# Optimization experiments

Measured on AMD Instinct MI355X. Metric: run time of the kernel, lower is better.

## Reference

```python
import jax, jax.numpy as jnp
import numpy as np

N_NODES = 100000
N_EDGES = 1600000
D = 128


def sage_conv(x, src, dst, W_l, b_l, W_r):
    # mean aggregation of neighbor features: messages flow src -> dst
    msgs = x[src]                                           # [E, D] gather
    agg = jax.ops.segment_sum(msgs, dst, num_segments=x.shape[0])  # [N, D]
    deg = jax.ops.segment_sum(jnp.ones((src.shape[0],), x.dtype), dst,
                              num_segments=x.shape[0])       # [N]
    agg = agg / jnp.maximum(deg, 1.0)[:, None]
    # PyG SAGEConv: lin_l(aggregated) + lin_r(root); bias lives in lin_l
    return agg @ W_l.T + b_l + x @ W_r.T


def setup_inputs() -> dict:
    key = jax.random.key(0)
    ks = jax.random.split(key, 8)
    s = 1.0 / np.sqrt(D)
    return {
        "x": jax.random.normal(ks[0], (N_NODES, D), dtype=jnp.float32),
        "edge_index": jax.random.randint(ks[1], (2, N_EDGES), 0, N_NODES, dtype=jnp.int64),
        "W1_l": jax.random.normal(ks[2], (D, D), dtype=jnp.float32) * s,
        "b1": jnp.zeros((D,), dtype=jnp.float32),
        "W1_r": jax.random.normal(ks[3], (D, D), dtype=jnp.float32) * s,
        "W2_l": jax.random.normal(ks[4], (D, D), dtype=jnp.float32) * s,
        "b2": jnp.zeros((D,), dtype=jnp.float32),
        "W2_r": jax.random.normal(ks[5], (D, D), dtype=jnp.float32) * s,
    }


def reference(x, edge_index, W1_l, b1, W1_r, W2_l, b2, W2_r):
    src, dst = edge_index[0], edge_index[1]
    h = jax.nn.relu(sage_conv(x, src, dst, W1_l, b1, W1_r))
    out = sage_conv(h, src, dst, W2_l, b2, W2_r)
    return out
```

## Files before the change

kernel.cpp:

```cpp
#include <hip/hip_runtime.h>
#include <cstdint>
#include <cstddef>

#define D 128

typedef unsigned short ushort_t;
typedef unsigned int uint_t;
typedef __attribute__((ext_vector_type(8))) short bf16x8;
typedef __attribute__((ext_vector_type(4))) float f32x4;

static __device__ __forceinline__ unsigned short f2bf(float f) {
    unsigned int u = __float_as_uint(f);
    u = (u + 0x7FFFu + ((u >> 16) & 1u)) >> 16;
    return (unsigned short)u;
}
static __device__ __forceinline__ float bf_lo(uint_t v) {
    return __uint_as_float(v << 16);
}
static __device__ __forceinline__ float bf_hi(uint_t v) {
    return __uint_as_float(v & 0xFFFF0000u);
}

static __device__ __forceinline__ void cast8(const float* __restrict__ s,
                                             ushort_t* __restrict__ d) {
    float4 a = *(const float4*)s;
    float4 b = *(const float4*)(s + 4);
    uint4 o;
    o.x = (uint_t)f2bf(a.x) | ((uint_t)f2bf(a.y) << 16);
    o.y = (uint_t)f2bf(a.z) | ((uint_t)f2bf(a.w) << 16);
    o.z = (uint_t)f2bf(b.x) | ((uint_t)f2bf(b.y) << 16);
    o.w = (uint_t)f2bf(b.z) | ((uint_t)f2bf(b.w) << 16);
    *(uint4*)d = o;
}


__global__ __launch_bounds__(256) void front_fused(
    const int* __restrict__ dst, int* __restrict__ bhist, int E, int EB,
    const float* __restrict__ x, ushort_t* __restrict__ xb, long nx, int CX,
    const float* __restrict__ W1l, const float* __restrict__ W1r,
    const float* __restrict__ W2l, const float* __restrict__ W2r,
    ushort_t* __restrict__ W1lb, ushort_t* __restrict__ W1rb,
    ushort_t* __restrict__ W2lb, ushort_t* __restrict__ W2rb) {
    __shared__ int lh[512];
    int b = blockIdx.x, t = threadIdx.x;
    if (b < EB) {
        lh[t] = 0;
        lh[t + 256] = 0;
        __syncthreads();
        int base = b * 4096;
#pragma unroll
        for (int i = 0; i < 16; ++i) {
            int e = base + i * 256 + t;
            if (e < E) atomicAdd(&lh[dst[e] >> 8], 1);
        }
        __syncthreads();
        if (lh[t]) atomicAdd(&bhist[t], lh[t]);
        if (lh[t + 256]) atomicAdd(&bhist[t + 256], lh[t + 256]);
    } else if (b < EB + CX) {
        long i = ((long)(b - EB) * 256 + t) * 8;
        if (i < nx) cast8(x + i, xb + i);
    } else {
        int bb = b - EB - CX;
        int arr = bb >> 3;
        long i = ((long)(bb & 7) * 256 + t) * 8;
        const float* s = (arr == 0) ? W1l : (arr == 1) ? W1r
                       : (arr == 2) ? W2l : W2r;
        ushort_t* d = (arr == 0) ? W1lb : (arr == 1) ? W1rb
                    : (arr == 2) ? W2lb : W2rb;
        cast8(s + i, d + i);
    }
}


__global__ __launch_bounds__(512) void bkt_scan(const int* __restrict__ bhist,
                                                int* __restrict__ boff,
                                                int* __restrict__ bcur,
                                                int* __restrict__ row_ptr,
                                                int N, int E) {
    __shared__ int s[512];
    int t = threadIdx.x;
    int v = bhist[t];
    s[t] = v;
    __syncthreads();
    for (int off = 1; off < 512; off <<= 1) {
        int u = (t >= off) ? s[t - off] : 0;
        __syncthreads();
        s[t] += u;
        __syncthreads();
    }
    int ex = s[t] - v;
    boff[t] = ex;
    bcur[t] = ex;
    if (t == 511) boff[512] = s[511];
    if (t == 0) row_ptr[N] = E;
}

__global__ __launch_bounds__(256) void bkt_scatter(const int* __restrict__ src,
                                                   const int* __restrict__ dst,
                                                   int* __restrict__ bcur,
                                                   int* __restrict__ ebuf, int E) {
    __shared__ int lh[512];
    __shared__ int lofs[512];
    __shared__ int gb[512];
    __shared__ int sv[4096];
    __shared__ unsigned short sb[4096];
    int t = threadIdx.x;
    lh[t] = 0;
    lh[t + 256] = 0;
    __syncthreads();
    int base = blockIdx.x * 4096;
    unsigned pk[16];
#pragma unroll
    for (int i = 0; i < 16; ++i) {
        int e = base + i * 256 + t;
        unsigned p = 0xFFFFFFFFu;
        if (e < E) {
            int d = dst[e];
            int bkt = d >> 8;
            int r = atomicAdd(&lh[bkt], 1);
            p = ((unsigned)r << 17) | ((unsigned)bkt << 8) | (unsigned)(d & 255);
        }
        pk[i] = p;
    }
    __syncthreads();
    int a0 = lh[2 * t], a1 = lh[2 * t + 1];
    int ps = a0 + a1;
    gb[t] = ps;
    __syncthreads();
    for (int off = 1; off < 256; off <<= 1) {
        int u = (t >= off) ? gb[t - off] : 0;
        __syncthreads();
        gb[t] += u;
        __syncthreads();
    }
    int inc = gb[t];
    int exb = inc - ps;
    __syncthreads();
    lofs[2 * t] = exb;
    lofs[2 * t + 1] = exb + a0;
    if (a0) gb[2 * t] = atomicAdd(&bcur[2 * t], a0);
    if (a1) gb[2 * t + 1] = atomicAdd(&bcur[2 * t + 1], a1);
    __syncthreads();
#pragma unroll
    for (int i = 0; i < 16; ++i) {
        int e = base + i * 256 + t;
        if (e < E) {
            unsigned p = pk[i];
            int bkt = (p >> 8) & 511;
            int r = (int)(p >> 17);
            int pos = lofs[bkt] + r;
            sv[pos] = src[e] | ((int)(p & 255) << 20);
            sb[pos] = (unsigned short)bkt;
        }
    }
    __syncthreads();
    int cnt = min(E - base, 4096);
    for (int i = t; i < cnt; i += 256) {
        int b2 = sb[i];
        ebuf[gb[b2] + (i - lofs[b2])] = sv[i];
    }
}

__global__ __launch_bounds__(256) void bkt_build(const int* __restrict__ ebuf,
                                                 const int* __restrict__ boff,
                                                 int* __restrict__ row_ptr,
                                                 int* __restrict__ csr, int N) {
    __shared__ int lcnt[256];
    __shared__ int lofs[256];
    __shared__ int lcur[256];
    int t = threadIdx.x;
    int b = blockIdx.x;
    int base = b << 8;
    int ebeg = boff[b], eend = boff[b + 1];
    lcnt[t] = 0;
    __syncthreads();
    for (int e = ebeg + t; e < eend; e += 256)
        atomicAdd(&lcnt[((unsigned)ebuf[e]) >> 20], 1);
    __syncthreads();
    int v = lcnt[t];
    lofs[t] = v;
    __syncthreads();
    for (int off = 1; off < 256; off <<= 1) {
        int u = (t >= off) ? lofs[t - off] : 0;
        __syncthreads();
        lofs[t] += u;
        __syncthreads();
    }
    int ex = lofs[t] - v;
    __syncthreads();
    lofs[t] = ex;
    lcur[t] = 0;
    if (base + t < N) row_ptr[base + t] = ebeg + ex;
    __syncthreads();
    for (int e = ebeg + t; e < eend; e += 256) {
        int u = ebuf[e];
        int d = ((unsigned)u) >> 20;
        int r = atomicAdd(&lcur[d], 1);
        csr[ebeg + lofs[d] + r] = u & 0xFFFFF;
    }
}


static __device__ __forceinline__ void acc8(uint4 v, float a[8]) {
    a[0] += bf_lo(v.x); a[1] += bf_hi(v.x);
    a[2] += bf_lo(v.y); a[3] += bf_hi(v.y);
    a[4] += bf_lo(v.z); a[5] += bf_hi(v.z);
    a[6] += bf_lo(v.w); a[7] += bf_hi(v.w);
}

static __device__ __forceinline__ uint4 grow(const ushort_t* __restrict__ xin,
                                             int s, int l16) {
    unsigned off = ((unsigned)s << 8) | ((unsigned)l16 << 4);
    return *(const uint4*)((const char*)xin + off);
}

static __device__ __forceinline__ void agg_store(ushort_t* __restrict__ aggb,
                                                 int node, int l16,
                                                 const float a[8], int deg) {
    float inv = 1.0f / fmaxf((float)deg, 1.0f);
    uint4 o;
    o.x = (uint_t)f2bf(a[0] * inv) | ((uint_t)f2bf(a[1] * inv) << 16);
    o.y = (uint_t)f2bf(a[2] * inv) | ((uint_t)f2bf(a[3] * inv) << 16);
    o.z = (uint_t)f2bf(a[4] * inv) | ((uint_t)f2bf(a[5] * inv) << 16);
    o.w = (uint_t)f2bf(a[6] * inv) | ((uint_t)f2bf(a[7] * inv) << 16);
    unsigned off = ((unsigned)node << 8) | ((unsigned)l16 << 4);
    *(uint4*)((char*)aggb + off) = o;
}

static __device__ __forceinline__ void agg_body(int bid, int base, int cnt,
                                                const ushort_t* __restrict__ xin,
                                                const int* __restrict__ csr,
                                                const int* __restrict__ row_ptr,
                                                ushort_t* __restrict__ aggb) {
    int wave = threadIdx.x >> 6;
    int lane = threadIdx.x & 63;
    int g = lane >> 4;
    int l16 = lane & 15;
    int p = bid * 8 + wave * 2;
    if (p >= cnt) return;
    int node0 = base + p;
    int node1 = base + min(p + 1, cnt - 1);
    int b0 = row_ptr[node0];
    int deg0 = row_ptr[node0 + 1] - b0;
    int b1 = row_ptr[node1];
    int deg1 = row_ptr[node1 + 1] - b1;
    int d0 = min(deg0, 64), d1 = min(deg1, 64);
    int i0 = (deg0 > 0) ? csr[b0 + min(lane, deg0 - 1)] : 0;
    int i1 = (deg1 > 0) ? csr[b1 + min(lane, deg1 - 1)] : 0;
    int c0 = max(d0 - 1, 0), c1 = max(d1 - 1, 0);
    float a0[8] = {0.f, 0.f, 0.f, 0.f, 0.f, 0.f, 0.f, 0.f};
    float a1[8] = {0.f, 0.f, 0.f, 0.f, 0.f, 0.f, 0.f, 0.f};
    int mm = max(d0, d1);
    for (int e = 0; e < mm; e += 16) {
        bool do0 = (e < d0), do1 = (e < d1);
        uint4 v0[4], v1[4];
        if (do0) {
#pragma unroll
            for (int q = 0; q < 4; ++q) {
                int s = __shfl(i0, min(e + 4 * q + g, c0));
                v0[q] = grow(xin, s, l16);
            }
        }
        if (do1) {
#pragma unroll
            for (int q = 0; q < 4; ++q) {
                int s = __shfl(i1, min(e + 4 * q + g, c1));
                v1[q] = grow(xin, s, l16);
            }
        }
        if (do0) {
#pragma unroll
            for (int q = 0; q < 4; ++q)
                if (e + 4 * q + g < d0) acc8(v0[q], a0);
        }
        if (do1) {
#pragma unroll
            for (int q = 0; q < 4; ++q)
                if (e + 4 * q + g < d1) acc8(v1[q], a1);
        }
    }
    for (int e2 = 64; e2 < deg0; e2 += 4) {
        int s = csr[b0 + min(e2 + g, deg0 - 1)];
        uint4 v = grow(xin, s, l16);
        if (e2 + g < deg0) acc8(v, a0);
    }
    for (int e2 = 64; e2 < deg1; e2 += 4) {
        int s = csr[b1 + min(e2 + g, deg1 - 1)];
        uint4 v = grow(xin, s, l16);
        if (e2 + g < deg1) acc8(v, a1);
    }
#pragma unroll
    for (int i = 0; i < 8; ++i) {
        a0[i] += __shfl_xor(a0[i], 16);
        a1[i] += __shfl_xor(a1[i], 16);
        a0[i] += __shfl_xor(a0[i], 32);
        a1[i] += __shfl_xor(a1[i], 32);
    }
    if (g == 0) {
        agg_store(aggb, node0, l16, a0, deg0);
        agg_store(aggb, node1, l16, a1, deg1);
    }
}

__global__ __launch_bounds__(256) void agg_k(const ushort_t* __restrict__ xin,
                                             const int* __restrict__ csr,
                                             const int* __restrict__ row_ptr,
                                             ushort_t* __restrict__ aggb,
                                             int base, int cnt) {
    agg_body(blockIdx.x, base, cnt, xin, csr, row_ptr, aggb);
}


static __device__ __forceinline__ void gemm_body(int tile, int rbase,
                                                 const ushort_t* __restrict__ Aagg,
                                                 const ushort_t* __restrict__ Ax,
                                                 const ushort_t* __restrict__ Wl,
                                                 const ushort_t* __restrict__ Wr,
                                                 const float* __restrict__ bias,
                                                 ushort_t* __restrict__ out_bf,
                                                 float* __restrict__ out_f32,
                                                 int N, int relu_bf) {
    __shared__ ushort_t sA[128 * 32];
    __shared__ ushort_t sW[128 * 32];
    int tid = threadIdx.x;
    int wave = tid >> 6, lane = tid & 63;
    int quad = lane >> 4, l15 = lane & 15;
    int wm = wave & 1, wc = wave >> 1;
    int n0 = rbase + tile * 128;
    int sr = tid >> 2;
    int sseg = (tid & 3) * 8;

    f32x4 acc[4][4];
#pragma unroll
    for (int mt = 0; mt < 4; ++mt)
#pragma unroll
        for (int nt = 0; nt < 4; ++nt) acc[mt][nt] = (f32x4){0.f, 0.f, 0.f, 0.f};

    int ga0 = min(n0 + sr, N - 1);
    int ga1 = min(n0 + sr + 64, N - 1);

#pragma unroll
    for (int c = 0; c < 8; ++c) {
        const ushort_t* Ab = (c < 4) ? Aagg : Ax;
        const ushort_t* Wb = (c < 4) ? Wl : Wr;
        int koff = (c & 3) * 32 + sseg;
        bf16x8 va0 = *(const bf16x8*)(Ab + (size_t)ga0 * D + koff);
        bf16x8 va1 = *(const bf16x8*)(Ab + (size_t)ga1 * D + koff);
        bf16x8 vw0 = *(const bf16x8*)(Wb + (size_t)sr * D + koff);
        bf16x8 vw1 = *(const bf16x8*)(Wb + (size_t)(sr + 64) * D + koff);
        __syncthreads();
        *(bf16x8*)&sA[sr * 32 + sseg] = va0;
        *(bf16x8*)&sA[(sr + 64) * 32 + sseg] = va1;
        *(bf16x8*)&sW[sr * 32 + sseg] = vw0;
        *(bf16x8*)&sW[(sr + 64) * 32 + sseg] = vw1;
        __syncthreads();

        bf16x8 af[4], wf[4];
#pragma unroll
        for (int mt = 0; mt < 4; ++mt)
            af[mt] = *(const bf16x8*)&sA[(wm * 64 + mt * 16 + l15) * 32 + quad * 8];
#pragma unroll
        for (int nt = 0; nt < 4; ++nt)
            wf[nt] = *(const bf16x8*)&sW[(wc * 64 + nt * 16 + l15) * 32 + quad * 8];
#pragma unroll
        for (int mt = 0; mt < 4; ++mt)
#pragma unroll
            for (int nt = 0; nt < 4; ++nt)
                acc[mt][nt] = __builtin_amdgcn_mfma_f32_16x16x32_bf16(
                    af[mt], wf[nt], acc[mt][nt], 0, 0, 0);
    }

#pragma unroll
    for (int mt = 0; mt < 4; ++mt) {
#pragma unroll
        for (int nt = 0; nt < 4; ++nt) {
            int col = wc * 64 + nt * 16 + l15;
            float bv = bias[col];
#pragma unroll
            for (int reg = 0; reg < 4; ++reg) {
                int row = n0 + wm * 64 + mt * 16 + quad * 4 + reg;
                if (row < N) {
                    float v = acc[mt][nt][reg] + bv;
                    if (relu_bf) {
                        v = fmaxf(v, 0.f);
                        out_bf[(size_t)row * D + col] = f2bf(v);
                    } else {
                        out_f32[(size_t)row * D + col] = v;
                    }
                }
            }
        }
    }
}

__global__ __launch_bounds__(256) void gemm_k(const ushort_t* __restrict__ Aagg,
                                              const ushort_t* __restrict__ Ax,
                                              const ushort_t* __restrict__ Wl,
                                              const ushort_t* __restrict__ Wr,
                                              const float* __restrict__ bias,
                                              ushort_t* __restrict__ out_bf,
                                              float* __restrict__ out_f32,
                                              int rbase, int N, int relu_bf) {
    gemm_body(blockIdx.x, rbase, Aagg, Ax, Wl, Wr, bias, out_bf, out_f32, N, relu_bf);
}

__global__ __launch_bounds__(256) void mid_fused(
    const ushort_t* __restrict__ xin, const int* __restrict__ csr,
    const int* __restrict__ row_ptr, ushort_t* __restrict__ aggb,
    const ushort_t* __restrict__ Wl, const ushort_t* __restrict__ Wr,
    const float* __restrict__ bias, ushort_t* __restrict__ out_bf,
    float* __restrict__ out_f32, int H, int N, int relu_bf, int aggBlocks) {
    if ((int)blockIdx.x < aggBlocks) {
        agg_body(blockIdx.x, H, N - H, xin, csr, row_ptr, aggb);
    } else {
        gemm_body(blockIdx.x - aggBlocks, 0, aggb, xin, Wl, Wr, bias,
                  out_bf, out_f32, N, relu_bf);
    }
}


extern "C" void kernel_launch(void* const* d_in, const int* in_sizes, int n_in,
                              void* d_out, int out_size, void* d_ws, size_t ws_size,
                              hipStream_t stream) {
    const float* x   = (const float*)d_in[0];
    const int*   ei  = (const int*)d_in[1];
    const float* W1l = (const float*)d_in[2];
    const float* b1  = (const float*)d_in[3];
    const float* W1r = (const float*)d_in[4];
    const float* W2l = (const float*)d_in[5];
    const float* b2  = (const float*)d_in[6];
    const float* W2r = (const float*)d_in[7];
    float* out = (float*)d_out;

    int N = in_sizes[0] / D;
    int E = in_sizes[1] / 2;
    const int* src = ei;
    const int* dst = ei + E;

    char* ws = (char*)d_ws;
    size_t off = 0;
    auto take = [&](size_t bytes) -> char* {
        char* p = ws + off;
        off += (bytes + 255) & ~(size_t)255;
        return p;
    };
    int*      row_ptr = (int*)take((size_t)(N + 1) * sizeof(int));
    int*      bhist   = (int*)take((size_t)(512 + 512 + 513) * sizeof(int));
    int*      bcur    = bhist + 512;
    int*      boff    = bhist + 1024;
    int*      ebuf    = (int*)take((size_t)E * sizeof(int));
    int*      csr     = (int*)take((size_t)E * sizeof(int));
    ushort_t* xb      = (ushort_t*)take((size_t)N * D * sizeof(ushort_t));
    ushort_t* hb      = (ushort_t*)take((size_t)N * D * sizeof(ushort_t));
    ushort_t* aggb    = (ushort_t*)take((size_t)N * D * sizeof(ushort_t));
    ushort_t* W1lb    = (ushort_t*)take((size_t)D * D * sizeof(ushort_t));
    ushort_t* W1rb    = (ushort_t*)take((size_t)D * D * sizeof(ushort_t));
    ushort_t* W2lb    = (ushort_t*)take((size_t)D * D * sizeof(ushort_t));
    ushort_t* W2rb    = (ushort_t*)take((size_t)D * D * sizeof(ushort_t));
    (void)ws_size;
    (void)n_in;
    (void)out_size;

    hipMemsetAsync(bhist, 0, 1024 * sizeof(int), stream);

    int NB = (N + 255) / 256;
    int EB = (E + 4095) / 4096;
    long nx = (long)N * D;
    int CX = (int)((nx / 8 + 255) / 256);

    front_fused<<<EB + CX + 32, 256, 0, stream>>>(
        dst, bhist, E, EB, x, xb, nx, CX,
        W1l, W1r, W2l, W2r, W1lb, W1rb, W2lb, W2rb);
    bkt_scan<<<1, 512, 0, stream>>>(bhist, boff, bcur, row_ptr, N, E);
    bkt_scatter<<<EB, 256, 0, stream>>>(src, dst, bcur, ebuf, E);
    bkt_build<<<NB, 256, 0, stream>>>(ebuf, boff, row_ptr, csr, N);

    int H = ((N / 2 + 127) / 128) * 128;
    if (H > N) H = N;
    int aggA = (H + 7) / 8;
    int aggB = (N - H + 7) / 8;
    int gemA = H / 128;
    int gemB = (N - H + 127) / 128;

    if (aggA) agg_k<<<aggA, 256, 0, stream>>>(xb, csr, row_ptr, aggb, 0, H);
    if (aggB + gemA)
        mid_fused<<<aggB + gemA, 256, 0, stream>>>(xb, csr, row_ptr, aggb,
                                                   W1lb, W1rb, b1, hb, nullptr,
                                                   H, N, 1, aggB);
    if (gemB) gemm_k<<<gemB, 256, 0, stream>>>(aggb, xb, W1lb, W1rb, b1,
                                               hb, nullptr, H, N, 1);

    if (aggA) agg_k<<<aggA, 256, 0, stream>>>(hb, csr, row_ptr, aggb, 0, H);
    if (aggB + gemA)
        mid_fused<<<aggB + gemA, 256, 0, stream>>>(hb, csr, row_ptr, aggb,
                                                   W2lb, W2rb, b2, nullptr, out,
                                                   H, N, 0, aggB);
    if (gemB) gemm_k<<<gemB, 256, 0, stream>>>(aggb, hb, W2lb, W2rb, b2,
                                               nullptr, out, H, N, 0);
}
```

Baseline: 367.0 us.

## Fold bucket scan into scatter/build kernels and drop split agg-gemm overlap

Removes the single-block bucket prefix-scan kernel. The scatter and build kernels now each recompute the global bucket offsets from the histogram, and the scatter kernel adds its atomic cursor on top of those offsets. The aggregation/GEMM split that overlapped half the aggregation with GEMM in a fused launch is replaced by one full aggregation kernel followed by one GEMM kernel per layer. This cuts launches and serial tiny-kernel gaps, at the cost of redundant per-block scans and the loss of agg/GEMM overlap.

```diff
diff --git a/kernel.cpp b/kernel.cpp
--- a/kernel.cpp
+++ b/kernel.cpp
@@ -40,9 +40,11 @@
     const float* __restrict__ W1l, const float* __restrict__ W1r,
     const float* __restrict__ W2l, const float* __restrict__ W2r,
     ushort_t* __restrict__ W1lb, ushort_t* __restrict__ W1rb,
-    ushort_t* __restrict__ W2lb, ushort_t* __restrict__ W2rb) {
+    ushort_t* __restrict__ W2lb, ushort_t* __restrict__ W2rb,
+    int* __restrict__ row_ptr, int N) {
     __shared__ int lh[512];
     int b = blockIdx.x, t = threadIdx.x;
+    if (b == 0 && t == 0) row_ptr[N] = E;
     if (b < EB) {
         lh[t] = 0;
         lh[t + 256] = 0;
@@ -72,36 +74,16 @@
 }
 
 
-__global__ __launch_bounds__(512) void bkt_scan(const int* __restrict__ bhist,
-                                                int* __restrict__ boff,
-                                                int* __restrict__ bcur,
-                                                int* __restrict__ row_ptr,
-                                                int N, int E) {
-    __shared__ int s[512];
-    int t = threadIdx.x;
-    int v = bhist[t];
-    s[t] = v;
-    __syncthreads();
-    for (int off = 1; off < 512; off <<= 1) {
-        int u = (t >= off) ? s[t - off] : 0;
-        __syncthreads();
-        s[t] += u;
-        __syncthreads();
-    }
-    int ex = s[t] - v;
-    boff[t] = ex;
-    bcur[t] = ex;
-    if (t == 511) boff[512] = s[511];
-    if (t == 0) row_ptr[N] = E;
-}
-
-__global__ __launch_bounds__(256) void bkt_scatter(const int* __restrict__ src,
-                                                   const int* __restrict__ dst,
-                                                   int* __restrict__ bcur,
-                                                   int* __restrict__ ebuf, int E) {
+__global__ __launch_bounds__(256) void bkt_scatter2(const int* __restrict__ src,
+                                                    const int* __restrict__ dst,
+                                                    const int* __restrict__ bhist,
+                                                    int* __restrict__ bcur,
+                                                    int* __restrict__ ebuf, int E) {
     __shared__ int lh[512];
     __shared__ int lofs[512];
-    __shared__ int gb[512];
+    __shared__ int gbs[512];
+    __shared__ int tA[256];
+    __shared__ int tB[256];
     __shared__ int sv[4096];
     __shared__ unsigned short sb[4096];
     int t = threadIdx.x;
@@ -124,22 +106,28 @@
     }
     __syncthreads();
     int a0 = lh[2 * t], a1 = lh[2 * t + 1];
-    int ps = a0 + a1;
-    gb[t] = ps;
+    int g0 = bhist[2 * t], g1 = bhist[2 * t + 1];
+    int ps = a0 + a1, gs = g0 + g1;
+    tA[t] = ps;
+    tB[t] = gs;
     __syncthreads();
     for (int off = 1; off < 256; off <<= 1) {
-        int u = (t >= off) ? gb[t - off] : 0;
-        __syncthreads();
-        gb[t] += u;
-        __syncthreads();
-    }
-    int inc = gb[t];
-    int exb = inc - ps;
-    __syncthreads();
-    lofs[2 * t] = exb;
-    lofs[2 * t + 1] = exb + a0;
-    if (a0) gb[2 * t] = atomicAdd(&bcur[2 * t], a0);
-    if (a1) gb[2 * t + 1] = atomicAdd(&bcur[2 * t + 1], a1);
+        int u1 = (t >= off) ? tA[t - off] : 0;
+        int u2 = (t >= off) ? tB[t - off] : 0;
+        __syncthreads();
+        tA[t] += u1;
+        tB[t] += u2;
+        __syncthreads();
+    }
+    int lexb = tA[t] - ps;
+    int gexb = tB[t] - gs;
+    lofs[2 * t] = lexb;
+    lofs[2 * t + 1] = lexb + a0;
+    gbs[2 * t] = gexb;
+    gbs[2 * t + 1] = gexb + g0;
+    __syncthreads();
+    if (a0) gbs[2 * t] += atomicAdd(&bcur[2 * t], a0);
+    if (a1) gbs[2 * t + 1] += atomicAdd(&bcur[2 * t + 1], a1);
     __syncthreads();
 #pragma unroll
     for (int i = 0; i < 16; ++i) {
@@ -157,23 +145,39 @@
     int cnt = min(E - base, 4096);
     for (int i = t; i < cnt; i += 256) {
         int b2 = sb[i];
-        ebuf[gb[b2] + (i - lofs[b2])] = sv[i];
-    }
-}
-
-__global__ __launch_bounds__(256) void bkt_build(const int* __restrict__ ebuf,
-                                                 const int* __restrict__ boff,
-                                                 int* __restrict__ row_ptr,
-                                                 int* __restrict__ csr, int N) {
+        ebuf[gbs[b2] + (i - lofs[b2])] = sv[i];
+    }
+}
+
+__global__ __launch_bounds__(256) void bkt_build2(const int* __restrict__ ebuf,
+                                                  const int* __restrict__ bhist,
+                                                  int* __restrict__ row_ptr,
+                                                  int* __restrict__ csr, int N) {
+    __shared__ int scn[512];
+    __shared__ int tA[256];
     __shared__ int lcnt[256];
     __shared__ int lofs[256];
     __shared__ int lcur[256];
     int t = threadIdx.x;
     int b = blockIdx.x;
     int base = b << 8;
-    int ebeg = boff[b], eend = boff[b + 1];
+    int g0 = bhist[2 * t], g1 = bhist[2 * t + 1];
+    int gs = g0 + g1;
+    tA[t] = gs;
+    __syncthreads();
+    for (int off = 1; off < 256; off <<= 1) {
+        int u = (t >= off) ? tA[t - off] : 0;
+        __syncthreads();
+        tA[t] += u;
+        __syncthreads();
+    }
+    int gexb = tA[t] - gs;
+    scn[2 * t] = gexb;
+    scn[2 * t + 1] = gexb + g0;
     lcnt[t] = 0;
     __syncthreads();
+    int ebeg = scn[b];
+    int eend = ebeg + bhist[b];
     for (int e = ebeg + t; e < eend; e += 256)
         atomicAdd(&lcnt[((unsigned)ebuf[e]) >> 20], 1);
     __syncthreads();
@@ -227,19 +231,18 @@
     *(uint4*)((char*)aggb + off) = o;
 }
 
-static __device__ __forceinline__ void agg_body(int bid, int base, int cnt,
-                                                const ushort_t* __restrict__ xin,
-                                                const int* __restrict__ csr,
-                                                const int* __restrict__ row_ptr,
-                                                ushort_t* __restrict__ aggb) {
+__global__ __launch_bounds__(256) void agg_k2(const ushort_t* __restrict__ xin,
+                                              const int* __restrict__ csr,
+                                              const int* __restrict__ row_ptr,
+                                              ushort_t* __restrict__ aggb, int N) {
     int wave = threadIdx.x >> 6;
     int lane = threadIdx.x & 63;
     int g = lane >> 4;
     int l16 = lane & 15;
-    int p = bid * 8 + wave * 2;
-    if (p >= cnt) return;
-    int node0 = base + p;
-    int node1 = base + min(p + 1, cnt - 1);
+    int p = blockIdx.x * 8 + wave * 2;
+    if (p >= N) return;
+    int node0 = p;
+    int node1 = min(p + 1, N - 1);
     int b0 = row_ptr[node0];
     int deg0 = row_ptr[node0 + 1] - b0;
     int b1 = row_ptr[node1];
@@ -302,17 +305,8 @@
     }
 }
 
-__global__ __launch_bounds__(256) void agg_k(const ushort_t* __restrict__ xin,
-                                             const int* __restrict__ csr,
-                                             const int* __restrict__ row_ptr,
-                                             ushort_t* __restrict__ aggb,
-                                             int base, int cnt) {
-    agg_body(blockIdx.x, base, cnt, xin, csr, row_ptr, aggb);
-}
-
-
-static __device__ __forceinline__ void gemm_body(int tile, int rbase,
-                                                 const ushort_t* __restrict__ Aagg,
+
+__global__ __launch_bounds__(256) void gemm_mfma(const ushort_t* __restrict__ Aagg,
                                                  const ushort_t* __restrict__ Ax,
                                                  const ushort_t* __restrict__ Wl,
                                                  const ushort_t* __restrict__ Wr,
@@ -326,7 +320,7 @@
     int wave = tid >> 6, lane = tid & 63;
     int quad = lane >> 4, l15 = lane & 15;
     int wm = wave & 1, wc = wave >> 1;
-    int n0 = rbase + tile * 128;
+    int n0 = blockIdx.x * 128;
     int sr = tid >> 2;
     int sseg = (tid & 3) * 8;
 
@@ -393,31 +387,6 @@
     }
 }
 
-__global__ __launch_bounds__(256) void gemm_k(const ushort_t* __restrict__ Aagg,
-                                              const ushort_t* __restrict__ Ax,
-                                              const ushort_t* __restrict__ Wl,
-                                              const ushort_t* __restrict__ Wr,
-                                              const float* __restrict__ bias,
-                                              ushort_t* __restrict__ out_bf,
-                                              float* __restrict__ out_f32,
-                                              int rbase, int N, int relu_bf) {
-    gemm_body(blockIdx.x, rbase, Aagg, Ax, Wl, Wr, bias, out_bf, out_f32, N, relu_bf);
-}
-
-__global__ __launch_bounds__(256) void mid_fused(
-    const ushort_t* __restrict__ xin, const int* __restrict__ csr,
-    const int* __restrict__ row_ptr, ushort_t* __restrict__ aggb,
-    const ushort_t* __restrict__ Wl, const ushort_t* __restrict__ Wr,
-    const float* __restrict__ bias, ushort_t* __restrict__ out_bf,
-    float* __restrict__ out_f32, int H, int N, int relu_bf, int aggBlocks) {
-    if ((int)blockIdx.x < aggBlocks) {
-        agg_body(blockIdx.x, H, N - H, xin, csr, row_ptr, aggb);
-    } else {
-        gemm_body(blockIdx.x - aggBlocks, 0, aggb, xin, Wl, Wr, bias,
-                  out_bf, out_f32, N, relu_bf);
-    }
-}
-
 
 extern "C" void kernel_launch(void* const* d_in, const int* in_sizes, int n_in,
                               void* d_out, int out_size, void* d_ws, size_t ws_size,
@@ -447,7 +416,6 @@
     int*      row_ptr = (int*)take((size_t)(N + 1) * sizeof(int));
     int*      bhist   = (int*)take((size_t)(512 + 512 + 513) * sizeof(int));
     int*      bcur    = bhist + 512;
-    int*      boff    = bhist + 1024;
     int*      ebuf    = (int*)take((size_t)E * sizeof(int));
     int*      csr     = (int*)take((size_t)E * sizeof(int));
     ushort_t* xb      = (ushort_t*)take((size_t)N * D * sizeof(ushort_t));
@@ -470,31 +438,16 @@
 
     front_fused<<<EB + CX + 32, 256, 0, stream>>>(
         dst, bhist, E, EB, x, xb, nx, CX,
-        W1l, W1r, W2l, W2r, W1lb, W1rb, W2lb, W2rb);
-    bkt_scan<<<1, 512, 0, stream>>>(bhist, boff, bcur, row_ptr, N, E);
-    bkt_scatter<<<EB, 256, 0, stream>>>(src, dst, bcur, ebuf, E);
-    bkt_build<<<NB, 256, 0, stream>>>(ebuf, boff, row_ptr, csr, N);
-
-    int H = ((N / 2 + 127) / 128) * 128;
-    if (H > N) H = N;
-    int aggA = (H + 7) / 8;
-    int aggB = (N - H + 7) / 8;
-    int gemA = H / 128;
-    int gemB = (N - H + 127) / 128;
-
-    if (aggA) agg_k<<<aggA, 256, 0, stream>>>(xb, csr, row_ptr, aggb, 0, H);
-    if (aggB + gemA)
-        mid_fused<<<aggB + gemA, 256, 0, stream>>>(xb, csr, row_ptr, aggb,
-                                                   W1lb, W1rb, b1, hb, nullptr,
-                                                   H, N, 1, aggB);
-    if (gemB) gemm_k<<<gemB, 256, 0, stream>>>(aggb, xb, W1lb, W1rb, b1,
-                                               hb, nullptr, H, N, 1);
-
-    if (aggA) agg_k<<<aggA, 256, 0, stream>>>(hb, csr, row_ptr, aggb, 0, H);
-    if (aggB + gemA)
-        mid_fused<<<aggB + gemA, 256, 0, stream>>>(hb, csr, row_ptr, aggb,
-                                                   W2lb, W2rb, b2, nullptr, out,
-                                                   H, N, 0, aggB);
-    if (gemB) gemm_k<<<gemB, 256, 0, stream>>>(aggb, hb, W2lb, W2rb, b2,
-                                               nullptr, out, H, N, 0);
-}
+        W1l, W1r, W2l, W2r, W1lb, W1rb, W2lb, W2rb, row_ptr, N);
+    bkt_scatter2<<<EB, 256, 0, stream>>>(src, dst, bhist, bcur, ebuf, E);
+    bkt_build2<<<NB, 256, 0, stream>>>(ebuf, bhist, row_ptr, csr, N);
+
+    int ablocks = (N + 7) / 8;
+    int gblocks = (N + 127) / 128;
+
+    agg_k2<<<ablocks, 256, 0, stream>>>(xb, csr, row_ptr, aggb, N);
+    gemm_mfma<<<gblocks, 256, 0, stream>>>(aggb, xb, W1lb, W1rb, b1, hb, nullptr, N, 1);
+
+    agg_k2<<<ablocks, 256, 0, stream>>>(hb, csr, row_ptr, aggb, N);
+    gemm_mfma<<<gblocks, 256, 0, stream>>>(aggb, hb, W2lb, W2rb, b2, nullptr, out, N, 0);
+}
```

After: 332.3 us. 9.5% less time.
